# Performance work log

Hardware: AMD Instinct MI355X
Metric: run time of the kernel (lower is better)

## Reference

```python
import jax, jax.numpy as jnp
import numpy as np

B, T, N = 16, 256, 20000
REGIONS, TOPK = 20000, 0.2
IN_DIM = int(REGIONS * TOPK ** 2)   # 800
K = int(REGIONS * TOPK)             # 4000
R = 1000                            # rest_limitation
ZCOLS = K + R                       # all-False mask columns per sample


def setup_inputs() -> dict:
    key = jax.random.key(0)
    ks = jax.random.split(key, 8)
    x = jax.random.normal(ks[0], (B, T, IN_DIM), jnp.float32)
    # first ZCOLS voxel columns are never covered (mask False), rest are covered
    border_mask = jnp.concatenate(
        [jnp.zeros((B, T, ZCOLS), bool), jnp.ones((B, T, N - ZCOLS), bool)], axis=-1)
    # K distinct indices per sample, drawn from the uncovered columns [0, ZCOLS)
    index = jax.vmap(lambda k: jax.random.permutation(k, ZCOLS)[:K])(
        jax.random.split(ks[1], B)).astype(jnp.int32)
    s1 = 1.0 / np.sqrt(IN_DIM); s2 = 1.0 / np.sqrt(K)
    W1 = jax.random.uniform(ks[2], (IN_DIM, K), jnp.float32, -s1, s1)
    b1 = jax.random.uniform(ks[3], (K,), jnp.float32, -s1, s1)
    W2 = jax.random.uniform(ks[4], (K, K), jnp.float32, -s2, s2)
    b2 = jax.random.uniform(ks[5], (K,), jnp.float32, -s2, s2)
    W3 = jax.random.uniform(ks[6], (K, R), jnp.float32, -s2, s2)
    b3 = jax.random.uniform(ks[7], (R,), jnp.float32, -s2, s2)
    return dict(x=x, border_mask=border_mask, index=index,
                W1=W1, b1=b1, W2=W2, b2=b2, W3=W3, b3=b3)


def reference(x, border_mask, index, W1, b1, W2, b2, W3, b3):
    h = x @ W1 + b1                  # unzip   [B,T,K]
    h = h @ W2 + b2                  # unprocess [B,T,K]
    x_rest = h @ W3 + b3             # rest    [B,T,R]
    colsum = border_mask.sum(axis=1)                 # [B,N] per-voxel coverage count
    idx_member = jax.vmap(lambda i: jnp.zeros((N,), bool).at[i].set(True))(index)
    # scatter h into indexed voxel columns
    x_recon = jax.vmap(lambda i, hb: jnp.zeros((T, N), h.dtype).at[:, i].set(hb))(index, h)
    # rest positions: uncovered columns not already taken by index (sorted order)
    rest_mask = (colsum == 0) & ~idx_member          # [B,N]
    rank = jnp.cumsum(rest_mask, axis=-1) - 1        # position among rest columns
    valid = rest_mask & (rank < R)                   # cap at rest_limitation ('adjust')
    g = jnp.take_along_axis(
        x_rest, jnp.broadcast_to(jnp.clip(rank, 0, R - 1)[:, None, :], (B, T, N)), axis=-1)
    return jnp.where(valid[:, None, :], g, x_recon)
```

## Files before the change

kernel.cpp:

```cpp
#include <hip/hip_runtime.h>

typedef __attribute__((ext_vector_type(4))) float f32x4;
typedef __attribute__((ext_vector_type(8))) __bf16 bf16x8;

#define B_SZ   16
#define T_SZ   256
#define BT_SZ  4096
#define N_VOX  20000
#define INDIM  800
#define K1P    896
#define K_DIM  4000
#define KP     4096
#define R_DIM  1000
#define RP     1024
#define SPLITK 4

__device__ __forceinline__ unsigned short f2bf(float f) {
  unsigned int u = __builtin_bit_cast(unsigned int, f);
  u += 0x7fffu + ((u >> 16) & 1u);
  return (unsigned short)(u >> 16);
}
__device__ __forceinline__ float bf2f(unsigned short h) {
  unsigned int u = ((unsigned int)h) << 16;
  return __builtin_bit_cast(float, u);
}
__device__ __forceinline__ void gload16(const void* g, void* l) {
  __builtin_amdgcn_global_load_lds(
      (const __attribute__((address_space(1))) void*)g,
      (__attribute__((address_space(3))) void*)l, 16, 0, 0);
}

#define PREP_CVT    4096
#define PREP_W1     3584
#define PREP_W2     16384
#define PREP_W3     4096
#define PREP_COV    320

__device__ void dev_transpose(const float* __restrict__ W,
                              unsigned short* __restrict__ WT,
                              int K, int N, int Kpad, int Npad,
                              int kb, int nb, int tx, int ty,
                              float (*tile)[33]) {
  int k0 = kb * 32, n0 = nb * 32;
  for (int i = ty; i < 32; i += 8) {
    int k = k0 + i, n = n0 + tx;
    tile[i][tx] = (k < K && n < N) ? W[(size_t)k * N + n] : 0.f;
  }
  __syncthreads();
  for (int i = ty; i < 32; i += 8) {
    int n = n0 + i, k = k0 + tx;
    if (n < Npad && k < Kpad)
      WT[(size_t)n * Kpad + k] = f2bf(tile[tx][i]);
  }
}

__global__ __launch_bounds__(256) void prep_kernel(
    const float* __restrict__ x, unsigned short* __restrict__ xb,
    const float* __restrict__ W1, unsigned short* __restrict__ w1t,
    const float* __restrict__ W2, unsigned short* __restrict__ w2t,
    const float* __restrict__ W3, unsigned short* __restrict__ w3t,
    const int* __restrict__ bmask, unsigned char* __restrict__ cov) {
  __shared__ float tile[32][33];
  int id = blockIdx.x;
  const int tid = threadIdx.x;
  const int tx = tid & 31, ty = tid >> 5;

  if (id < PREP_CVT) {
    int row = id, c4 = tid;
    if (c4 < K1P / 4) {
      ushort4 o = {0, 0, 0, 0};
      if (c4 < INDIM / 4) {
        float4 v = ((const float4*)(x + (size_t)row * INDIM))[c4];
        o.x = f2bf(v.x); o.y = f2bf(v.y); o.z = f2bf(v.z); o.w = f2bf(v.w);
      }
      ((ushort4*)(xb + (size_t)row * K1P))[c4] = o;
    }
    return;
  }
  id -= PREP_CVT;
  if (id < PREP_W1) {
    dev_transpose(W1, w1t, INDIM, K_DIM, K1P, KP, id % 28, id / 28, tx, ty, tile);
    return;
  }
  id -= PREP_W1;
  if (id < PREP_W2) {
    dev_transpose(W2, w2t, K_DIM, K_DIM, KP, KP, id % 128, id / 128, tx, ty, tile);
    return;
  }
  id -= PREP_W2;
  if (id < PREP_W3) {
    dev_transpose(W3, w3t, K_DIM, R_DIM, KP, RP, id % 128, id / 128, tx, ty, tile);
    return;
  }
  id -= PREP_W3;
  {
    int n4 = (id % 20) * 256 + tid;
    int b = id / 20;
    if (n4 >= N_VOX / 4) return;
    const int4* p = (const int4*)(bmask + (size_t)b * T_SZ * N_VOX) + n4;
    int4 a = {0, 0, 0, 0};
    for (int t0 = 0; t0 < T_SZ; t0 += 8) {
      int4 c[8];
#pragma unroll
      for (int tt = 0; tt < 8; ++tt)
        c[tt] = p[(size_t)(t0 + tt) * (N_VOX / 4)];
#pragma unroll
      for (int tt = 0; tt < 8; ++tt) {
        a.x |= c[tt].x; a.y |= c[tt].y; a.z |= c[tt].z; a.w |= c[tt].w;
      }
      if (a.x && a.y && a.z && a.w) break;
    }
    uchar4 o;
    o.x = (unsigned char)(a.x != 0); o.y = (unsigned char)(a.y != 0);
    o.z = (unsigned char)(a.z != 0); o.w = (unsigned char)(a.w != 0);
    *(uchar4*)(cov + (size_t)b * N_VOX + (size_t)n4 * 4) = o;
  }
}

__global__ void map_kernel(const int* __restrict__ index,
                           const unsigned char* __restrict__ cov,
                           int* __restrict__ srcmap) {
  int b = blockIdx.x, tid = threadIdx.x;
  int* sm = srcmap + (size_t)b * N_VOX;
  for (int n = tid; n < N_VOX; n += 1024) sm[n] = -1;
  __syncthreads();
  const int* idx = index + (size_t)b * K_DIM;
  for (int j = tid; j < K_DIM; j += 1024) sm[idx[j]] = j;
  __syncthreads();

  __shared__ int wsum[16];
  __shared__ int s_running;
  if (tid == 0) s_running = 0;
  __syncthreads();
  const int lane = tid & 63, wid = tid >> 6;
  const unsigned char* cv = cov + (size_t)b * N_VOX;
  for (int base = 0; base < N_VOX; base += 1024) {
    int n = base + tid;
    bool flag = (n < N_VOX) && (!cv[n]) && (sm[n] < 0);
    unsigned long long bal = __ballot(flag);
    if (lane == 0) wsum[wid] = __popcll(bal);
    __syncthreads();
    int woff = 0, tot = 0;
    for (int w = 0; w < 16; ++w) {
      int c = wsum[w];
      if (w < wid) woff += c;
      tot += c;
    }
    int rank = s_running + woff + __popcll(bal & ((1ull << lane) - 1ull));
    if (flag && rank < R_DIM) sm[n] = K_DIM + rank;
    __syncthreads();
    if (tid == 0) s_running += tot;
    __syncthreads();
  }
}

template <int BM, bool SPLIT>
__global__ __launch_bounds__(256) void gemm_bt(
    const unsigned short* __restrict__ A,
    const unsigned short* __restrict__ BTm,
    const float* __restrict__ bias, int nbias,
    unsigned short* __restrict__ C,
    int K, int lda, int ldb, int ldc, size_t zstride) {
  constexpr int MI = BM / 32;
  __shared__ __align__(16) unsigned short As[BM * 32];
  __shared__ __align__(16) unsigned short Bs[128 * 32];
  const int tid = threadIdx.x;
  const int wid = tid >> 6;
  const int lane = tid & 63;
  const int bm = blockIdx.y, bn = blockIdx.x;
  if (SPLIT) {
    int kz = blockIdx.z;
    A += (size_t)kz * K;
    BTm += (size_t)kz * K;
    C += (size_t)kz * zstride;
  }
  const int wm = wid >> 1, wn = wid & 1;
  const int sub = lane >> 2;
  const int quad = lane & 3;

  const int rA0 = wid * 16 + sub;
  const char* gA0 = (const char*)(A + (size_t)(bm * BM + rA0) * lda) + quad * 16;
  const char* gA1 = (const char*)(A + (size_t)(bm * BM + ((BM == 128) ? rA0 + 64 : rA0)) * lda) + quad * 16;
  const char* gB0 = (const char*)(BTm + (size_t)(bn * 128 + rA0) * ldb) + quad * 16;
  const char* gB1 = (const char*)(BTm + (size_t)(bn * 128 + rA0 + 64) * ldb) + quad * 16;

  char* lA0 = (char*)As + wid * 1024 + lane * 16;
  char* lA1 = lA0 + 4096;
  char* lB0 = (char*)Bs + wid * 1024 + lane * 16;
  char* lB1 = lB0 + 4096;

  const int r15 = lane & 15;
  const int kg = lane >> 4;

  f32x4 acc[MI][4] = {};

  for (int kt = 0; kt < K; kt += 32) {
    const int kb = kt * 2;
    gload16(gA0 + kb, lA0);
    if constexpr (BM == 128) gload16(gA1 + kb, lA1);
    gload16(gB0 + kb, lB0);
    gload16(gB1 + kb, lB1);
    __syncthreads();
    bf16x8 af[MI], bfr[4];
#pragma unroll
    for (int i = 0; i < MI; ++i)
      af[i] = *(const bf16x8*)&As[(wm * (BM / 2) + i * 16 + r15) * 32 + kg * 8];
#pragma unroll
    for (int j = 0; j < 4; ++j)
      bfr[j] = *(const bf16x8*)&Bs[(wn * 64 + j * 16 + r15) * 32 + kg * 8];
#pragma unroll
    for (int i = 0; i < MI; ++i)
#pragma unroll
      for (int j = 0; j < 4; ++j)
        acc[i][j] = __builtin_amdgcn_mfma_f32_16x16x32_bf16(af[i], bfr[j], acc[i][j], 0, 0, 0);
    __syncthreads();
  }

#pragma unroll
  for (int i = 0; i < MI; ++i) {
    const int row0 = bm * BM + wm * (BM / 2) + i * 16 + kg * 4;
#pragma unroll
    for (int j = 0; j < 4; ++j) {
      const int col = bn * 128 + wn * 64 + j * 16 + r15;
      float bv = 0.f;
      if constexpr (!SPLIT) bv = bias[(col < nbias) ? col : (nbias - 1)];
#pragma unroll
      for (int r = 0; r < 4; ++r)
        C[(size_t)(row0 + r) * ldc + col] = f2bf(acc[i][j][r] + bv);
    }
  }
}

__global__ __launch_bounds__(512, 2) void gemm256(
    const unsigned short* __restrict__ A,
    const unsigned short* __restrict__ BTm,
    const float* __restrict__ bias, int nbias,
    unsigned short* __restrict__ C,
    int K, int lda, int ldb, int ldc) {
  __shared__ __align__(16) char smem[131072];
  const int tid = threadIdx.x;
  const int wid = tid >> 6, lane = tid & 63;
  const int wm = wid >> 2, wn = wid & 3;
  const int r15 = lane & 15, kg = lane >> 4;
  const int bm = blockIdx.y, bn = blockIdx.x;

  const int srow = tid >> 2;
  const int scol = ((tid & 3) * 8) ^ ((srow & 8) ? 16 : 0);
  const unsigned short* gA = A + (size_t)(bm * 256 + srow) * lda + scol;
  const unsigned short* gB = BTm + (size_t)(bn * 256 + srow) * ldb + scol;

  const int cxor = (kg * 16) ^ ((r15 & 8) ? 32 : 0);
  const int aoff = (wm * 128 + r15) * 64 + cxor;
  const int boff = (wn * 64 + r15) * 64 + cxor;

  f32x4 acc[8][4] = {};
  bf16x8 bfr[4];

#define STAGE_HALF(S, MAT, KH, TN)                                            \
  {                                                                           \
    const unsigned short* g =                                                 \
        ((MAT) ? gB : gA) + (size_t)(TN) * 64 + (KH) * 32;                    \
    char* l = smem + (S) * 65536 + (MAT) * 32768 + (KH) * 16384 + tid * 16;   \
    gload16(g, l);                                                            \
    gload16(g + (size_t)128 * ((MAT) ? ldb : lda), l + 8192);                 \
  }

#define PHASE(S, KS, MH, TN, DOVM)                                            \
  {                                                                           \
    bf16x8 af[4];                                                             \
    if ((MH) == 0) {                                                          \
      _Pragma("unroll")                                                       \
      for (int j = 0; j < 4; ++j)                                             \
        bfr[j] = *(const bf16x8*)(smem + (S) * 65536 + 32768 +                \
                                  (KS) * 16384 + boff + j * 1024);            \
    }                                                                         \
    _Pragma("unroll")                                                         \
    for (int i = 0; i < 4; ++i)                                               \
      af[i] = *(const bf16x8*)(smem + (S) * 65536 + (KS) * 16384 +            \
                               (MH) * 4096 + aoff + i * 1024);                \
    STAGE_HALF((S) ^ 1, (MH), (KS), TN)                                       \
    if (DOVM) asm volatile("s_waitcnt vmcnt(4)" ::: "memory");                \
    asm volatile("s_barrier" ::: "memory");                                   \
    __builtin_amdgcn_s_setprio(1);                                            \
    _Pragma("unroll")                                                         \
    for (int i = 0; i < 4; ++i)                                               \
      _Pragma("unroll")                                                       \
      for (int j = 0; j < 4; ++j)                                             \
        acc[(MH) * 4 + i][j] = __builtin_amdgcn_mfma_f32_16x16x32_bf16(       \
            af[i], bfr[j], acc[(MH) * 4 + i][j], 0, 0, 0);                    \
    __builtin_amdgcn_s_setprio(0);                                            \
    asm volatile("s_barrier" ::: "memory");                                   \
  }

#define TILE4(S, TN)                                                          \
  PHASE(S, 0, 0, TN, 0)                                                       \
  PHASE(S, 0, 1, TN, 1)                                                       \
  PHASE(S, 1, 0, TN, 0)                                                       \
  PHASE(S, 1, 1, TN, 1)

  const int NT = K >> 6;
  STAGE_HALF(0, 0, 0, 0)
  STAGE_HALF(0, 1, 0, 0)
  STAGE_HALF(0, 0, 1, 0)
  STAGE_HALF(0, 1, 1, 0)
  asm volatile("s_waitcnt vmcnt(4)" ::: "memory");
  asm volatile("s_barrier" ::: "memory");

  for (int tp = 0; tp < NT; tp += 2) {
    const int tn1 = tp + 1;
    TILE4(0, tn1)
    const int tn2 = (tp + 2 < NT) ? tp + 2 : NT - 1;
    TILE4(1, tn2)
  }

#undef STAGE_HALF
#undef PHASE
#undef TILE4

#pragma unroll
  for (int f = 0; f < 8; ++f) {
    const int row0 = bm * 256 + wm * 128 + f * 16 + kg * 4;
#pragma unroll
    for (int j = 0; j < 4; ++j) {
      const int col = bn * 256 + wn * 64 + j * 16 + r15;
      const float bv = bias[(col < nbias) ? col : (nbias - 1)];
#pragma unroll
      for (int r = 0; r < 4; ++r)
        C[(size_t)(row0 + r) * ldc + col] = f2bf(acc[f][j][r] + bv);
    }
  }
}

__global__ void fill_out(const int* __restrict__ srcmap,
                         const unsigned short* __restrict__ h2b,
                         const unsigned short* __restrict__ xpart,
                         const float* __restrict__ b3,
                         float* __restrict__ out) {
  int n4 = blockIdx.x * 256 + threadIdx.x;
  if (n4 >= N_VOX / 4) return;
  int t = blockIdx.y, b = blockIdx.z;
  size_t bt = (size_t)b * T_SZ + t;
  const int4 sm = ((const int4*)(srcmap + (size_t)b * N_VOX))[n4];
  const unsigned short* hrow = h2b + bt * KP;
  const unsigned short* xrow = xpart + bt * RP;
  const size_t zs = (size_t)BT_SZ * RP;
  auto val = [&](int s) -> float {
    if (s < 0) return 0.f;
    if (s < K_DIM) return bf2f(hrow[s]);
    int r = s - K_DIM;
    float acc = b3[r];
#pragma unroll
    for (int z = 0; z < SPLITK; ++z) acc += bf2f(xrow[z * zs + r]);
    return acc;
  };
  f32x4 v;
  v.x = val(sm.x); v.y = val(sm.y); v.z = val(sm.z); v.w = val(sm.w);
  __builtin_nontemporal_store(v, (f32x4*)(out + bt * N_VOX) + n4);
}

extern "C" void kernel_launch(void* const* d_in, const int* in_sizes, int n_in,
                              void* d_out, int out_size, void* d_ws, size_t ws_size,
                              hipStream_t stream) {
  const float* x          = (const float*)d_in[0];
  const int* bm           = (const int*)d_in[1];
  const int* index        = (const int*)d_in[2];
  const float* W1         = (const float*)d_in[3];
  const float* b1         = (const float*)d_in[4];
  const float* W2         = (const float*)d_in[5];
  const float* b2         = (const float*)d_in[6];
  const float* W3         = (const float*)d_in[7];
  const float* b3         = (const float*)d_in[8];
  float* out = (float*)d_out;

  char* ws = (char*)d_ws;
  size_t off = 0;
  auto alloc = [&](size_t bytes) -> void* {
    void* p = ws + off;
    off += (bytes + 255) & ~(size_t)255;
    return p;
  };
  unsigned short* xb    = (unsigned short*)alloc((size_t)BT_SZ * K1P * 2);
  unsigned short* w1t   = (unsigned short*)alloc((size_t)KP * K1P * 2);
  unsigned short* w2t   = (unsigned short*)alloc((size_t)KP * KP * 2);
  unsigned short* w3t   = (unsigned short*)alloc((size_t)RP * KP * 2);
  unsigned short* h1b   = (unsigned short*)alloc((size_t)BT_SZ * KP * 2);
  unsigned short* h2b   = (unsigned short*)alloc((size_t)BT_SZ * KP * 2);
  unsigned short* xpart = (unsigned short*)alloc((size_t)SPLITK * BT_SZ * RP * 2);
  unsigned char* cov = (unsigned char*)alloc((size_t)B_SZ * N_VOX);
  int* srcmap = (int*)alloc((size_t)B_SZ * N_VOX * 4);

  {
    int nblk = PREP_CVT + PREP_W1 + PREP_W2 + PREP_W3 + PREP_COV;
    prep_kernel<<<nblk, 256, 0, stream>>>(x, xb, W1, w1t, W2, w2t, W3, w3t, bm, cov);
  }
  map_kernel<<<B_SZ, 1024, 0, stream>>>(index, cov, srcmap);

  {
    dim3 g(KP / 256, BT_SZ / 256);
    gemm256<<<g, 512, 0, stream>>>(xb, w1t, b1, K_DIM, h1b, K1P, K1P, K1P, KP);
  }
  {
    dim3 g(KP / 256, BT_SZ / 256);
    gemm256<<<g, 512, 0, stream>>>(h1b, w2t, b2, K_DIM, h2b, KP, KP, KP, KP);
  }
  {
    dim3 g(RP / 128, BT_SZ / 128, SPLITK);
    gemm_bt<128, true><<<g, 256, 0, stream>>>(h2b, w3t, nullptr, 0, xpart,
                                              KP / SPLITK, KP, KP, RP,
                                              (size_t)BT_SZ * RP);
  }

  {
    dim3 g((N_VOX / 4 + 255) / 256, T_SZ, B_SZ);
    fill_out<<<g, 256, 0, stream>>>(srcmap, h2b, xpart, b3, out);
  }
}
```

Measured before the change: 433.6 us.

## Reuse pipelined 256-tile GEMM for split-K third layer and batch fill_out over time

Removes the simple 128-tile gemm_bt kernel and templates the pipelined gemm256 kernel with a split-K mode, so the third GEMM (h2 @ W3) uses the larger double-buffered tiles with 4-way K split. The fill_out kernel now has each thread load its srcmap entry once and loop over 64 timesteps, instead of launching one block row per timestep. This is meant to speed up the third GEMM and cut redundant srcmap loads and launch overhead. The trade-off is fewer blocks (4x16x4 = 256) for GEMM3 and less parallelism in fill_out.

```diff
diff --git a/kernel.cpp b/kernel.cpp
--- a/kernel.cpp
+++ b/kernel.cpp
@@ -154,95 +154,25 @@
   }
 }
 
-template <int BM, bool SPLIT>
-__global__ __launch_bounds__(256) void gemm_bt(
+template <bool SPLIT>
+__global__ __launch_bounds__(512, 2) void gemm256(
     const unsigned short* __restrict__ A,
     const unsigned short* __restrict__ BTm,
     const float* __restrict__ bias, int nbias,
     unsigned short* __restrict__ C,
     int K, int lda, int ldb, int ldc, size_t zstride) {
-  constexpr int MI = BM / 32;
-  __shared__ __align__(16) unsigned short As[BM * 32];
-  __shared__ __align__(16) unsigned short Bs[128 * 32];
-  const int tid = threadIdx.x;
-  const int wid = tid >> 6;
-  const int lane = tid & 63;
-  const int bm = blockIdx.y, bn = blockIdx.x;
-  if (SPLIT) {
-    int kz = blockIdx.z;
-    A += (size_t)kz * K;
-    BTm += (size_t)kz * K;
-    C += (size_t)kz * zstride;
-  }
-  const int wm = wid >> 1, wn = wid & 1;
-  const int sub = lane >> 2;
-  const int quad = lane & 3;
-
-  const int rA0 = wid * 16 + sub;
-  const char* gA0 = (const char*)(A + (size_t)(bm * BM + rA0) * lda) + quad * 16;
-  const char* gA1 = (const char*)(A + (size_t)(bm * BM + ((BM == 128) ? rA0 + 64 : rA0)) * lda) + quad * 16;
-  const char* gB0 = (const char*)(BTm + (size_t)(bn * 128 + rA0) * ldb) + quad * 16;
-  const char* gB1 = (const char*)(BTm + (size_t)(bn * 128 + rA0 + 64) * ldb) + quad * 16;
-
-  char* lA0 = (char*)As + wid * 1024 + lane * 16;
-  char* lA1 = lA0 + 4096;
-  char* lB0 = (char*)Bs + wid * 1024 + lane * 16;
-  char* lB1 = lB0 + 4096;
-
-  const int r15 = lane & 15;
-  const int kg = lane >> 4;
-
-  f32x4 acc[MI][4] = {};
-
-  for (int kt = 0; kt < K; kt += 32) {
-    const int kb = kt * 2;
-    gload16(gA0 + kb, lA0);
-    if constexpr (BM == 128) gload16(gA1 + kb, lA1);
-    gload16(gB0 + kb, lB0);
-    gload16(gB1 + kb, lB1);
-    __syncthreads();
-    bf16x8 af[MI], bfr[4];
-#pragma unroll
-    for (int i = 0; i < MI; ++i)
-      af[i] = *(const bf16x8*)&As[(wm * (BM / 2) + i * 16 + r15) * 32 + kg * 8];
-#pragma unroll
-    for (int j = 0; j < 4; ++j)
-      bfr[j] = *(const bf16x8*)&Bs[(wn * 64 + j * 16 + r15) * 32 + kg * 8];
-#pragma unroll
-    for (int i = 0; i < MI; ++i)
-#pragma unroll
-      for (int j = 0; j < 4; ++j)
-        acc[i][j] = __builtin_amdgcn_mfma_f32_16x16x32_bf16(af[i], bfr[j], acc[i][j], 0, 0, 0);
-    __syncthreads();
-  }
-
-#pragma unroll
-  for (int i = 0; i < MI; ++i) {
-    const int row0 = bm * BM + wm * (BM / 2) + i * 16 + kg * 4;
-#pragma unroll
-    for (int j = 0; j < 4; ++j) {
-      const int col = bn * 128 + wn * 64 + j * 16 + r15;
-      float bv = 0.f;
-      if constexpr (!SPLIT) bv = bias[(col < nbias) ? col : (nbias - 1)];
-#pragma unroll
-      for (int r = 0; r < 4; ++r)
-        C[(size_t)(row0 + r) * ldc + col] = f2bf(acc[i][j][r] + bv);
-    }
-  }
-}
-
-__global__ __launch_bounds__(512, 2) void gemm256(
-    const unsigned short* __restrict__ A,
-    const unsigned short* __restrict__ BTm,
-    const float* __restrict__ bias, int nbias,
-    unsigned short* __restrict__ C,
-    int K, int lda, int ldb, int ldc) {
   __shared__ __align__(16) char smem[131072];
   const int tid = threadIdx.x;
   const int wid = tid >> 6, lane = tid & 63;
   const int wm = wid >> 2, wn = wid & 3;
   const int r15 = lane & 15, kg = lane >> 4;
   const int bm = blockIdx.y, bn = blockIdx.x;
+  if constexpr (SPLIT) {
+    const int kz = blockIdx.z;
+    A += (size_t)kz * K;
+    BTm += (size_t)kz * K;
+    C += (size_t)kz * zstride;
+  }
 
   const int srow = tid >> 2;
   const int scol = ((tid & 3) * 8) ^ ((srow & 8) ? 16 : 0);
@@ -323,7 +253,8 @@
 #pragma unroll
     for (int j = 0; j < 4; ++j) {
       const int col = bn * 256 + wn * 64 + j * 16 + r15;
-      const float bv = bias[(col < nbias) ? col : (nbias - 1)];
+      float bv = 0.f;
+      if constexpr (!SPLIT) bv = bias[(col < nbias) ? col : (nbias - 1)];
 #pragma unroll
       for (int r = 0; r < 4; ++r)
         C[(size_t)(row0 + r) * ldc + col] = f2bf(acc[f][j][r] + bv);
@@ -331,31 +262,37 @@
   }
 }
 
-__global__ void fill_out(const int* __restrict__ srcmap,
-                         const unsigned short* __restrict__ h2b,
-                         const unsigned short* __restrict__ xpart,
-                         const float* __restrict__ b3,
-                         float* __restrict__ out) {
-  int n4 = blockIdx.x * 256 + threadIdx.x;
-  if (n4 >= N_VOX / 4) return;
-  int t = blockIdx.y, b = blockIdx.z;
-  size_t bt = (size_t)b * T_SZ + t;
-  const int4 sm = ((const int4*)(srcmap + (size_t)b * N_VOX))[n4];
-  const unsigned short* hrow = h2b + bt * KP;
-  const unsigned short* xrow = xpart + bt * RP;
+__global__ __launch_bounds__(256) void fill_out(
+    const int* __restrict__ srcmap,
+    const unsigned short* __restrict__ h2b,
+    const unsigned short* __restrict__ xpart,
+    const float* __restrict__ b3,
+    float* __restrict__ out) {
+  const int n4 = blockIdx.x * 256 + threadIdx.x;
+  const int b = blockIdx.z;
+  const bool live = (n4 < N_VOX / 4);
+  int4 sm = {-1, -1, -1, -1};
+  if (live) sm = ((const int4*)(srcmap + (size_t)b * N_VOX))[n4];
   const size_t zs = (size_t)BT_SZ * RP;
-  auto val = [&](int s) -> float {
-    if (s < 0) return 0.f;
-    if (s < K_DIM) return bf2f(hrow[s]);
-    int r = s - K_DIM;
-    float acc = b3[r];
-#pragma unroll
-    for (int z = 0; z < SPLITK; ++z) acc += bf2f(xrow[z * zs + r]);
-    return acc;
-  };
-  f32x4 v;
-  v.x = val(sm.x); v.y = val(sm.y); v.z = val(sm.z); v.w = val(sm.w);
-  __builtin_nontemporal_store(v, (f32x4*)(out + bt * N_VOX) + n4);
+  const int t0 = blockIdx.y * 64;
+  for (int tt = 0; tt < 64; ++tt) {
+    const size_t bt = (size_t)b * T_SZ + t0 + tt;
+    if (!live) continue;
+    const unsigned short* hrow = h2b + bt * KP;
+    const unsigned short* xrow = xpart + bt * RP;
+    auto val = [&](int s) -> float {
+      if (s < 0) return 0.f;
+      if (s < K_DIM) return bf2f(hrow[s]);
+      int r = s - K_DIM;
+      float acc = b3[r];
+#pragma unroll
+      for (int z = 0; z < SPLITK; ++z) acc += bf2f(xrow[z * zs + r]);
+      return acc;
+    };
+    f32x4 v;
+    v.x = val(sm.x); v.y = val(sm.y); v.z = val(sm.z); v.w = val(sm.w);
+    __builtin_nontemporal_store(v, (f32x4*)(out + bt * N_VOX) + n4);
+  }
 }
 
 extern "C" void kernel_launch(void* const* d_in, const int* in_sizes, int n_in,
@@ -397,21 +334,23 @@
 
   {
     dim3 g(KP / 256, BT_SZ / 256);
-    gemm256<<<g, 512, 0, stream>>>(xb, w1t, b1, K_DIM, h1b, K1P, K1P, K1P, KP);
+    gemm256<false><<<g, 512, 0, stream>>>(xb, w1t, b1, K_DIM, h1b,
+                                          K1P, K1P, K1P, KP, 0);
   }
   {
     dim3 g(KP / 256, BT_SZ / 256);
-    gemm256<<<g, 512, 0, stream>>>(h1b, w2t, b2, K_DIM, h2b, KP, KP, KP, KP);
-  }
-  {
-    dim3 g(RP / 128, BT_SZ / 128, SPLITK);
-    gemm_bt<128, true><<<g, 256, 0, stream>>>(h2b, w3t, nullptr, 0, xpart,
-                                              KP / SPLITK, KP, KP, RP,
-                                              (size_t)BT_SZ * RP);
-  }
-
-  {
-    dim3 g((N_VOX / 4 + 255) / 256, T_SZ, B_SZ);
+    gemm256<false><<<g, 512, 0, stream>>>(h1b, w2t, b2, K_DIM, h2b,
+                                          KP, KP, KP, KP, 0);
+  }
+  {
+    dim3 g(RP / 256, BT_SZ / 256, SPLITK);
+    gemm256<true><<<g, 512, 0, stream>>>(h2b, w3t, nullptr, 0, xpart,
+                                         KP / SPLITK, KP, KP, RP,
+                                         (size_t)BT_SZ * RP);
+  }
+
+  {
+    dim3 g(N_VOX / 4 / 256 + 1, T_SZ / 64, B_SZ);
     fill_out<<<g, 256, 0, stream>>>(srcmap, h2b, xpart, b3, out);
   }
 }
```

Result: slower. 471.1 us (+8.6%).
